# Kernel optimization log

Hardware: AMD Instinct MI355X
Metric: run time of the kernel (lower is better)

## Reference

```python
import jax, jax.numpy as jnp
import numpy as np

V, E, B, T = 50000, 512, 8, 512

def setup_inputs() -> dict:
    key = jax.random.key(0)
    ks = jax.random.split(key, 9)
    s_ih = 1.0 / np.sqrt(E)
    return {
        "x": jax.random.randint(ks[0], (B, T), 0, V, dtype=jnp.int64),
        "y": jax.random.randint(ks[1], (B, T), 0, V, dtype=jnp.int64),
        "embedding": jax.random.normal(ks[2], (V, E), dtype=jnp.float32),
        "w_ih": jax.random.uniform(ks[3], (4 * E, E), jnp.float32, -s_ih, s_ih),
        "w_hh": jax.random.uniform(ks[4], (4 * E, E), jnp.float32, -s_ih, s_ih),
        "b_ih": jax.random.uniform(ks[5], (4 * E,), jnp.float32, -s_ih, s_ih),
        "b_hh": jax.random.uniform(ks[6], (4 * E,), jnp.float32, -s_ih, s_ih),
        "dec_w": jax.random.uniform(ks[7], (V, E), jnp.float32, -s_ih, s_ih),
        "dec_b": jax.random.uniform(ks[8], (V,), jnp.float32, -s_ih, s_ih),
    }

def _lstm(embed, w_ih, w_hh, b_ih, b_hh):
    # embed: [B, T, E]. Precompute input projections for all timesteps.
    xproj = jnp.einsum("bte,ge->btg", embed, w_ih) + b_ih  # [B, T, 4E]
    xproj = jnp.swapaxes(xproj, 0, 1)                      # [T, B, 4E]
    h0 = jnp.zeros((embed.shape[0], w_hh.shape[1]), embed.dtype)
    c0 = jnp.zeros_like(h0)

    def step(carry, xp_t):
        h, c = carry
        gates = xp_t + h @ w_hh.T + b_hh          # [B, 4E]
        i, f, g, o = jnp.split(gates, 4, axis=-1)  # PyTorch gate order: i,f,g,o
        i = jax.nn.sigmoid(i)
        f = jax.nn.sigmoid(f)
        g = jnp.tanh(g)
        o = jax.nn.sigmoid(o)
        c = f * c + i * g
        h = o * jnp.tanh(c)
        return (h, c), h

    _, hs = jax.lax.scan(step, (h0, c0), xproj)   # hs: [T, B, E]
    return jnp.swapaxes(hs, 0, 1)                 # [B, T, E]

def reference(x, y, embedding, w_ih, w_hh, b_ih, b_hh, dec_w, dec_b):
    embed = embedding[x]                                   # [B, T, E]
    lstm_out = _lstm(embed, w_ih, w_hh, b_ih, b_hh)        # [B, T, E]
    y_pred = jnp.einsum("bte,ve->btv", lstm_out, dec_w) + dec_b  # [B, T, V]
    return y_pred
```

## Files before the change

### kernel.cpp

```cpp
#include <hip/hip_runtime.h>
#include <hip/hip_bf16.h>
#include <stdint.h>

typedef short bf16x8 __attribute__((ext_vector_type(8)));
typedef float f32x4 __attribute__((ext_vector_type(4)));
typedef _Float16 half2v __attribute__((ext_vector_type(2)));

typedef const __attribute__((address_space(1))) unsigned int glob_u32;
typedef __attribute__((address_space(3))) unsigned int lds_u32;

__device__ __forceinline__ void gl_lds16(const void* g, void* s) {
  __builtin_amdgcn_global_load_lds((glob_u32*)g, (lds_u32*)s, 16, 0, 0);
}

__device__ __forceinline__ unsigned short f2bf(float f) {
  __hip_bfloat16 h = __float2bfloat16(f);
  return __builtin_bit_cast(unsigned short, h);
}
__device__ __forceinline__ float bf2f(unsigned short u) {
  __hip_bfloat16 h = __builtin_bit_cast(__hip_bfloat16, u);
  return __bfloat162float(h);
}

__device__ __forceinline__ float sigm_fast(float x) {
  float e = __expf(-x);
  return __builtin_amdgcn_rcpf(1.f + e);
}
__device__ __forceinline__ float tanh_fast(float x) {
  float e = __expf(2.f * x);
  return 1.f - 2.f * __builtin_amdgcn_rcpf(e + 1.f);
}

__device__ __forceinline__ float dot2(unsigned a, unsigned b, float acc) {
  return __builtin_amdgcn_fdot2(__builtin_bit_cast(half2v, a),
                                __builtin_bit_cast(half2v, b), acc, false);
}

__global__ void split_hl(const float* __restrict__ src,
                         unsigned short* __restrict__ hi,
                         unsigned short* __restrict__ lo, int n4) {
  int i = blockIdx.x * blockDim.x + threadIdx.x;
  if (i >= n4) return;
  float4 v = reinterpret_cast<const float4*>(src)[i];
  ushort4 h, l;
  h.x = f2bf(v.x); l.x = f2bf(v.x - bf2f(h.x));
  h.y = f2bf(v.y); l.y = f2bf(v.y - bf2f(h.y));
  h.z = f2bf(v.z); l.z = f2bf(v.z - bf2f(h.z));
  h.w = f2bf(v.w); l.w = f2bf(v.w - bf2f(h.w));
  reinterpret_cast<ushort4*>(hi)[i] = h;
  reinterpret_cast<ushort4*>(lo)[i] = l;
}

__global__ void split_h(const float* __restrict__ src,
                        unsigned short* __restrict__ hi, int n4) {
  int i = blockIdx.x * blockDim.x + threadIdx.x;
  if (i >= n4) return;
  float4 v = reinterpret_cast<const float4*>(src)[i];
  ushort4 h;
  h.x = f2bf(v.x); h.y = f2bf(v.y); h.z = f2bf(v.z); h.w = f2bf(v.w);
  reinterpret_cast<ushort4*>(hi)[i] = h;
}

__global__ void gather_split(const int* __restrict__ x, const float* __restrict__ emb,
                             unsigned short* __restrict__ hi,
                             unsigned short* __restrict__ lo) {
  int i = blockIdx.x * 256 + threadIdx.x;
  int m = i >> 7, k4 = i & 127;
  long row = x[m];
  float4 v = reinterpret_cast<const float4*>(emb + row * 512)[k4];
  ushort4 h, l;
  h.x = f2bf(v.x); l.x = f2bf(v.x - bf2f(h.x));
  h.y = f2bf(v.y); l.y = f2bf(v.y - bf2f(h.y));
  h.z = f2bf(v.z); l.z = f2bf(v.z - bf2f(h.z));
  h.w = f2bf(v.w); l.w = f2bf(v.w - bf2f(h.w));
  reinterpret_cast<ushort4*>(hi)[m * 128 + k4] = h;
  reinterpret_cast<ushort4*>(lo)[m * 128 + k4] = l;
}

__global__ __launch_bounds__(256) void gemm_split(
    const unsigned short* __restrict__ Ahi, const unsigned short* __restrict__ Alo,
    const unsigned short* __restrict__ Bhi, const unsigned short* __restrict__ Blo,
    float* __restrict__ C, const float* __restrict__ bias1,
    const float* __restrict__ bias2, int N, int mtiles) {
  __shared__ unsigned short lds[4][128 * 64];
  int nwg = gridDim.x;
  int wid = (blockIdx.x & 7) * (nwg >> 3) + (blockIdx.x >> 3);
  int mt = wid % mtiles, nt = wid / mtiles;
  int m0 = mt * 128, n0 = nt * 128;
  int tid = threadIdx.x, l = tid & 63, w = tid >> 6;
  int wm = (w & 1) * 64, wn = (w >> 1) * 64;

  f32x4 acc[4][4];
#pragma unroll
  for (int a = 0; a < 4; ++a)
#pragma unroll
    for (int b = 0; b < 4; ++b) acc[a][b] = f32x4{0.f, 0.f, 0.f, 0.f};

  const unsigned short* srcs[4] = {Ahi, Alo, Bhi, Blo};

  for (int kc = 0; kc < 8; ++kc) {
    __syncthreads();
#pragma unroll
    for (int tile = 0; tile < 4; ++tile) {
      const unsigned short* src = srcs[tile];
      int rbase = (tile < 2) ? m0 : n0;
#pragma unroll
      for (int i = 0; i < 4; ++i) {
        int G = (i * 4 + w) * 64 + l;
        int r = G >> 3, g = G & 7;
        int row = rbase + r;
        long gb = (long)row * 1024 + kc * 128 + ((g * 16) ^ ((r & 7) << 4));
        gl_lds16((const char*)src + gb, (char*)(&lds[tile][0]) + (i * 4 + w) * 1024);
      }
    }
    __syncthreads();

    const char* ldsb = (const char*)&lds[0][0];
#pragma unroll
    for (int ks = 0; ks < 2; ++ks) {
      bf16x8 ah[4], al[4], bh[4], bl[4];
      int biw = ks * 64 + ((l >> 4) * 16);
#pragma unroll
      for (int fm = 0; fm < 4; ++fm) {
        int row = wm + fm * 16 + (l & 15);
        int off = row * 128 + (biw ^ ((row & 7) << 4));
        ah[fm] = *reinterpret_cast<const bf16x8*>(ldsb + off);
        al[fm] = *reinterpret_cast<const bf16x8*>(ldsb + 16384 + off);
      }
#pragma unroll
      for (int fn = 0; fn < 4; ++fn) {
        int row = wn + fn * 16 + (l & 15);
        int off = row * 128 + (biw ^ ((row & 7) << 4));
        bh[fn] = *reinterpret_cast<const bf16x8*>(ldsb + 32768 + off);
        bl[fn] = *reinterpret_cast<const bf16x8*>(ldsb + 49152 + off);
      }
#pragma unroll
      for (int fm = 0; fm < 4; ++fm)
#pragma unroll
        for (int fn = 0; fn < 4; ++fn) {
          acc[fm][fn] = __builtin_amdgcn_mfma_f32_16x16x32_bf16(ah[fm], bh[fn], acc[fm][fn], 0, 0, 0);
          acc[fm][fn] = __builtin_amdgcn_mfma_f32_16x16x32_bf16(ah[fm], bl[fn], acc[fm][fn], 0, 0, 0);
          acc[fm][fn] = __builtin_amdgcn_mfma_f32_16x16x32_bf16(al[fm], bh[fn], acc[fm][fn], 0, 0, 0);
        }
    }
  }

#pragma unroll
  for (int fn = 0; fn < 4; ++fn) {
    int n = n0 + wn + fn * 16 + (l & 15);
    float bs = bias1[n];
    if (bias2) bs += bias2[n];
#pragma unroll
    for (int fm = 0; fm < 4; ++fm) {
      int mb = m0 + wm + fm * 16 + (l >> 4) * 4;
#pragma unroll
      for (int j = 0; j < 4; ++j)
        C[(long)(mb + j) * N + n] = acc[fm][fn][j] + bs;
    }
  }
}

__global__ __launch_bounds__(256) void gemm_plain(
    const unsigned short* __restrict__ Ahi, const unsigned short* __restrict__ Bhi,
    float* __restrict__ C, const float* __restrict__ bias1, int N) {
  __shared__ unsigned short lds[2][128 * 64];
  int xcd = blockIdx.x & 7;
  int wid = blockIdx.x >> 3;
  int mt = xcd * 4 + (wid & 3);
  int nt = wid >> 2;
  int m0 = mt * 128, n0 = nt * 128;
  int tid = threadIdx.x, l = tid & 63, w = tid >> 6;
  int wm = (w & 1) * 64, wn = (w >> 1) * 64;

  f32x4 acc[4][4];
#pragma unroll
  for (int a = 0; a < 4; ++a)
#pragma unroll
    for (int b = 0; b < 4; ++b) acc[a][b] = f32x4{0.f, 0.f, 0.f, 0.f};

  const unsigned short* srcs[2] = {Ahi, Bhi};

  for (int kc = 0; kc < 8; ++kc) {
    __syncthreads();
#pragma unroll
    for (int tile = 0; tile < 2; ++tile) {
      const unsigned short* src = srcs[tile];
      int rbase = (tile < 1) ? m0 : n0;
#pragma unroll
      for (int i = 0; i < 4; ++i) {
        int G = (i * 4 + w) * 64 + l;
        int r = G >> 3, g = G & 7;
        int row = rbase + r;
        if (tile == 1 && row >= N) row = n0;
        long gb = (long)row * 1024 + kc * 128 + ((g * 16) ^ ((r & 7) << 4));
        gl_lds16((const char*)src + gb, (char*)(&lds[tile][0]) + (i * 4 + w) * 1024);
      }
    }
    __syncthreads();

    const char* ldsb = (const char*)&lds[0][0];
#pragma unroll
    for (int ks = 0; ks < 2; ++ks) {
      bf16x8 ah[4], bh[4];
      int biw = ks * 64 + ((l >> 4) * 16);
#pragma unroll
      for (int fm = 0; fm < 4; ++fm) {
        int row = wm + fm * 16 + (l & 15);
        int off = row * 128 + (biw ^ ((row & 7) << 4));
        ah[fm] = *reinterpret_cast<const bf16x8*>(ldsb + off);
      }
#pragma unroll
      for (int fn = 0; fn < 4; ++fn) {
        int row = wn + fn * 16 + (l & 15);
        int off = row * 128 + (biw ^ ((row & 7) << 4));
        bh[fn] = *reinterpret_cast<const bf16x8*>(ldsb + 16384 + off);
      }
#pragma unroll
      for (int fm = 0; fm < 4; ++fm)
#pragma unroll
        for (int fn = 0; fn < 4; ++fn)
          acc[fm][fn] = __builtin_amdgcn_mfma_f32_16x16x32_bf16(ah[fm], bh[fn], acc[fm][fn], 0, 0, 0);
    }
  }

#pragma unroll
  for (int fn = 0; fn < 4; ++fn) {
    int n = n0 + wn + fn * 16 + (l & 15);
    if (n < N) {
      float bs = bias1[n];
#pragma unroll
      for (int fm = 0; fm < 4; ++fm) {
        int mb = m0 + wm + fm * 16 + (l >> 4) * 4;
#pragma unroll
        for (int j = 0; j < 4; ++j)
          C[(long)(mb + j) * N + n] = acc[fm][fn][j] + bs;
      }
    }
  }
}

__global__ __launch_bounds__(256, 1) void lstm_persistent(
    const float* __restrict__ xproj,
    const float* __restrict__ whh,
    float* lstm_f32,
    unsigned short* __restrict__ lstm_hi) {
  int bid = blockIdx.x;
  int batch = bid & 7, slice = bid >> 3;
  int tid = threadIdx.x, l = tid & 63, w = tid >> 6;
  int g = l >> 4, e = l & 15;
  long R = (long)g * 512 + slice * 16 + e;

  __shared__ unsigned hs_pk[256];
  __shared__ float part_s[2][4][64];

  unsigned wpk[64];
  {
    const float2* wp = reinterpret_cast<const float2*>(whh + R * 512 + w * 128);
#pragma unroll
    for (int jj = 0; jj < 64; ++jj) {
      float2 v = wp[jj];
      wpk[jj] = __builtin_bit_cast(unsigned, __builtin_amdgcn_cvt_pkrtz(v.x, v.y));
    }
  }
#pragma unroll
  for (int jj = 0; jj < 64; jj += 4)
    asm volatile("" : "+v"(wpk[jj]), "+v"(wpk[jj + 1]), "+v"(wpk[jj + 2]), "+v"(wpk[jj + 3]));

  const float* xbase = xproj + (long)batch * 512 * 2048 + g * 512 + slice * 16 + e;
  float* hrow_base = lstm_f32 + (long)batch * 512 * 512;
  float c_reg = 0.f;

  for (int t = 0; t < 512; ++t) {
    float xp = 0.f;
    if (w == 0) xp = xbase[(long)t * 2048];

    float a0 = 0.f, a1 = 0.f, a2 = 0.f, a3 = 0.f;
    if (t > 0) {
      const unsigned long long* src = reinterpret_cast<const unsigned long long*>(
          hrow_base + (long)(t - 1) * 512 + w * 128) + l;
      unsigned long long u = __hip_atomic_load(src, __ATOMIC_RELAXED, __HIP_MEMORY_SCOPE_AGENT);
      unsigned long long u2 = __hip_atomic_load(src, __ATOMIC_RELAXED, __HIP_MEMORY_SCOPE_AGENT);
      while ((unsigned)u == 0xFFFFFFFFu || (unsigned)(u >> 32) == 0xFFFFFFFFu) {
        u = u2;
        u2 = __hip_atomic_load(src, __ATOMIC_RELAXED, __HIP_MEMORY_SCOPE_AGENT);
      }
      float hx = __builtin_bit_cast(float, (unsigned)u);
      float hy = __builtin_bit_cast(float, (unsigned)(u >> 32));
      hs_pk[w * 64 + l] =
          __builtin_bit_cast(unsigned, __builtin_amdgcn_cvt_pkrtz(hx, hy));
      asm volatile("s_waitcnt lgkmcnt(0)" ::: "memory");
      __builtin_amdgcn_sched_barrier(0);
      const uint4* hv = reinterpret_cast<const uint4*>(&hs_pk[w * 64]);
#pragma unroll
      for (int jj = 0; jj < 16; ++jj) {
        uint4 q = hv[jj];
        a0 = dot2(wpk[jj * 4 + 0], q.x, a0);
        a1 = dot2(wpk[jj * 4 + 1], q.y, a1);
        a2 = dot2(wpk[jj * 4 + 2], q.z, a2);
        a3 = dot2(wpk[jj * 4 + 3], q.w, a3);
      }
    }
    part_s[t & 1][w][l] = (a0 + a1) + (a2 + a3);
    __syncthreads();

    if (w == 0) {
      float sum = xp + part_s[t & 1][0][l] + part_s[t & 1][1][l] +
                  part_s[t & 1][2][l] + part_s[t & 1][3][l];
      float val = (g == 2) ? tanh_fast(sum) : sigm_fast(sum);
      float vf = __shfl(val, e + 16);
      float vg = __shfl(val, e + 32);
      float vo = __shfl(val, e + 48);
      if (l < 16) {
        float c = vf * c_reg + val * vg;
        c_reg = c;
        float h = vo * tanh_fast(c);
        long oidx = ((long)batch * 512 + t) * 512 + slice * 16 + l;
        __hip_atomic_store(reinterpret_cast<unsigned int*>(lstm_f32) + oidx,
                           __builtin_bit_cast(unsigned int, h),
                           __ATOMIC_RELAXED, __HIP_MEMORY_SCOPE_AGENT);
        lstm_hi[oidx] = f2bf(h);
      }
    }
  }
}

extern "C" void kernel_launch(void* const* d_in, const int* in_sizes, int n_in,
                              void* d_out, int out_size, void* d_ws, size_t ws_size,
                              hipStream_t stream) {
  const int*   x         = (const int*)d_in[0];
  const float* embedding = (const float*)d_in[2];
  const float* w_ih      = (const float*)d_in[3];
  const float* w_hh      = (const float*)d_in[4];
  const float* b_ih      = (const float*)d_in[5];
  const float* b_hh      = (const float*)d_in[6];
  const float* dec_w     = (const float*)d_in[7];
  const float* dec_b     = (const float*)d_in[8];

  char* ws = (char*)d_ws;
  float* xproj = (float*)ws;                      ws += (size_t)4096 * 2048 * 4;
  float* lstmf = (float*)ws;                      ws += (size_t)4096 * 512 * 4;
  unsigned short* lstm_hi = (unsigned short*)ws;  ws += (size_t)4096 * 512 * 2;
  unsigned short* emb_hi  = (unsigned short*)ws;  ws += (size_t)4096 * 512 * 2;
  unsigned short* emb_lo  = (unsigned short*)ws;  ws += (size_t)4096 * 512 * 2;
  unsigned short* wih_hi  = (unsigned short*)ws;  ws += (size_t)2048 * 512 * 2;
  unsigned short* wih_lo  = (unsigned short*)ws;  ws += (size_t)2048 * 512 * 2;
  unsigned short* dw_hi   = (unsigned short*)ws;  ws += (size_t)50000 * 512 * 2;

  hipMemsetAsync(lstmf, 0xFF, (size_t)4096 * 512 * 4, stream);

  split_hl<<<1024, 256, 0, stream>>>(w_ih, wih_hi, wih_lo, 2048 * 512 / 4);
  split_h<<<25000, 256, 0, stream>>>(dec_w, dw_hi, 50000 * 512 / 4);
  gather_split<<<2048, 256, 0, stream>>>(x, embedding, emb_hi, emb_lo);

  gemm_split<<<32 * 16, 256, 0, stream>>>(emb_hi, emb_lo, wih_hi, wih_lo, xproj,
                                          b_ih, b_hh, 2048, 32);

  {
    void* args[] = {(void*)&xproj, (void*)&w_hh, (void*)&lstmf, (void*)&lstm_hi};
    hipLaunchCooperativeKernel((void*)lstm_persistent, dim3(256), dim3(256), args, 0, stream);
  }

  gemm_plain<<<32 * 391, 256, 0, stream>>>(lstm_hi, dw_hi, (float*)d_out, dec_b, 50000);
}
```

Measured before the change: 1.223 ms.

## Exchange LSTM hidden state as packed fp16 and remap decoder GEMM tiles per XCD

```diff
diff --git a/kernel.cpp b/kernel.cpp
--- a/kernel.cpp
+++ b/kernel.cpp
@@ -166,9 +166,10 @@
   __shared__ unsigned short lds[2][128 * 64];
   int xcd = blockIdx.x & 7;
   int wid = blockIdx.x >> 3;
-  int mt = xcd * 4 + (wid & 3);
-  int nt = wid >> 2;
+  int mt = (xcd & 1) * 16 + (wid & 15);
+  int nt = (xcd >> 1) * 98 + (wid >> 4);
   int m0 = mt * 128, n0 = nt * 128;
+  if (n0 >= N) return;
   int tid = threadIdx.x, l = tid & 63, w = tid >> 6;
   int wm = (w & 1) * 64, wn = (w >> 1) * 64;
 
@@ -242,7 +243,7 @@
 __global__ __launch_bounds__(256, 1) void lstm_persistent(
     const float* __restrict__ xproj,
     const float* __restrict__ whh,
-    float* lstm_f32,
+    unsigned* hpk,
     unsigned short* __restrict__ lstm_hi) {
   int bid = blockIdx.x;
   int batch = bid & 7, slice = bid >> 3;
@@ -267,8 +268,10 @@
     asm volatile("" : "+v"(wpk[jj]), "+v"(wpk[jj + 1]), "+v"(wpk[jj + 2]), "+v"(wpk[jj + 3]));
 
   const float* xbase = xproj + (long)batch * 512 * 2048 + g * 512 + slice * 16 + e;
-  float* hrow_base = lstm_f32 + (long)batch * 512 * 512;
+  unsigned* hrow_base = hpk + (long)batch * 512 * 256;
   float c_reg = 0.f;
+
+#define PL(p) __hip_atomic_load((p), __ATOMIC_RELAXED, __HIP_MEMORY_SCOPE_AGENT)
 
   for (int t = 0; t < 512; ++t) {
     float xp = 0.f;
@@ -276,18 +279,10 @@
 
     float a0 = 0.f, a1 = 0.f, a2 = 0.f, a3 = 0.f;
     if (t > 0) {
-      const unsigned long long* src = reinterpret_cast<const unsigned long long*>(
-          hrow_base + (long)(t - 1) * 512 + w * 128) + l;
-      unsigned long long u = __hip_atomic_load(src, __ATOMIC_RELAXED, __HIP_MEMORY_SCOPE_AGENT);
-      unsigned long long u2 = __hip_atomic_load(src, __ATOMIC_RELAXED, __HIP_MEMORY_SCOPE_AGENT);
-      while ((unsigned)u == 0xFFFFFFFFu || (unsigned)(u >> 32) == 0xFFFFFFFFu) {
-        u = u2;
-        u2 = __hip_atomic_load(src, __ATOMIC_RELAXED, __HIP_MEMORY_SCOPE_AGENT);
-      }
-      float hx = __builtin_bit_cast(float, (unsigned)u);
-      float hy = __builtin_bit_cast(float, (unsigned)(u >> 32));
-      hs_pk[w * 64 + l] =
-          __builtin_bit_cast(unsigned, __builtin_amdgcn_cvt_pkrtz(hx, hy));
+      const unsigned* src = hrow_base + (long)(t - 1) * 256 + w * 64 + l;
+      unsigned p0 = PL(src), p1 = PL(src), p2 = PL(src), p3 = PL(src);
+      while (p0 == 0xFFFFFFFFu) { p0 = p1; p1 = p2; p2 = p3; p3 = PL(src); }
+      hs_pk[w * 64 + l] = p0;
       asm volatile("s_waitcnt lgkmcnt(0)" ::: "memory");
       __builtin_amdgcn_sched_barrier(0);
       const uint4* hv = reinterpret_cast<const uint4*>(&hs_pk[w * 64]);
@@ -310,18 +305,24 @@
       float vf = __shfl(val, e + 16);
       float vg = __shfl(val, e + 32);
       float vo = __shfl(val, e + 48);
+      float hval = 0.f;
       if (l < 16) {
         float c = vf * c_reg + val * vg;
         c_reg = c;
-        float h = vo * tanh_fast(c);
+        hval = vo * tanh_fast(c);
         long oidx = ((long)batch * 512 + t) * 512 + slice * 16 + l;
-        __hip_atomic_store(reinterpret_cast<unsigned int*>(lstm_f32) + oidx,
-                           __builtin_bit_cast(unsigned int, h),
+        lstm_hi[oidx] = f2bf(hval);
+      }
+      float hup = __shfl(hval, l ^ 1);
+      if (l < 16 && !(l & 1)) {
+        unsigned pk = __builtin_bit_cast(unsigned,
+                        __builtin_amdgcn_cvt_pkrtz(hval, hup));
+        __hip_atomic_store(hrow_base + (long)t * 256 + slice * 8 + (l >> 1), pk,
                            __ATOMIC_RELAXED, __HIP_MEMORY_SCOPE_AGENT);
-        lstm_hi[oidx] = f2bf(h);
-      }
-    }
-  }
+      }
+    }
+  }
+#undef PL
 }
 
 extern "C" void kernel_launch(void* const* d_in, const int* in_sizes, int n_in,
@@ -338,7 +339,7 @@
 
   char* ws = (char*)d_ws;
   float* xproj = (float*)ws;                      ws += (size_t)4096 * 2048 * 4;
-  float* lstmf = (float*)ws;                      ws += (size_t)4096 * 512 * 4;
+  unsigned* hpk = (unsigned*)ws;                  ws += (size_t)4096 * 256 * 4;
   unsigned short* lstm_hi = (unsigned short*)ws;  ws += (size_t)4096 * 512 * 2;
   unsigned short* emb_hi  = (unsigned short*)ws;  ws += (size_t)4096 * 512 * 2;
   unsigned short* emb_lo  = (unsigned short*)ws;  ws += (size_t)4096 * 512 * 2;
@@ -346,7 +347,7 @@
   unsigned short* wih_lo  = (unsigned short*)ws;  ws += (size_t)2048 * 512 * 2;
   unsigned short* dw_hi   = (unsigned short*)ws;  ws += (size_t)50000 * 512 * 2;
 
-  hipMemsetAsync(lstmf, 0xFF, (size_t)4096 * 512 * 4, stream);
+  hipMemsetAsync(hpk, 0xFF, (size_t)4096 * 256 * 4, stream);
 
   split_hl<<<1024, 256, 0, stream>>>(w_ih, wih_hi, wih_lo, 2048 * 512 / 4);
   split_h<<<25000, 256, 0, stream>>>(dec_w, dw_hi, 50000 * 512 / 4);
@@ -356,9 +357,9 @@
                                           b_ih, b_hh, 2048, 32);
 
   {
-    void* args[] = {(void*)&xproj, (void*)&w_hh, (void*)&lstmf, (void*)&lstm_hi};
+    void* args[] = {(void*)&xproj, (void*)&w_hh, (void*)&hpk, (void*)&lstm_hi};
     hipLaunchCooperativeKernel((void*)lstm_persistent, dim3(256), dim3(256), args, 0, stream);
   }
 
-  gemm_plain<<<32 * 391, 256, 0, stream>>>(lstm_hi, dw_hi, (float*)d_out, dec_b, 50000);
-}
+  gemm_plain<<<8 * 1568, 256, 0, stream>>>(lstm_hi, dw_hi, (float*)d_out, dec_b, 50000);
+}
```

Result: slower. 1.655 ms (+35.4%).
